# Kernel tuning notes

Hardware: AMD Instinct MI355X
Metric: run time of the kernel (lower is better)

Reference implementation:

```python
import jax, jax.numpy as jnp
import numpy as np

B = 65536
IN_F = 512
OUT_F = 256
NUM_GROUPS = 8
EPS = 1e-5


def setup_inputs() -> dict:
    key = jax.random.key(0)
    ks = jax.random.split(key, 6)
    return {
        "x": jax.random.normal(ks[0], (B, IN_F), dtype=jnp.float32),
        "weight": jax.random.normal(ks[1], (OUT_F, IN_F), dtype=jnp.float32) * 0.05,
        "bias_linear": jax.random.normal(ks[2], (OUT_F,), dtype=jnp.float32) * 0.05,
        "weight_gn": jax.random.normal(ks[3], (OUT_F,), dtype=jnp.float32),
        "bias_gn": jax.random.normal(ks[4], (OUT_F,), dtype=jnp.float32),
        "bias": jax.random.normal(ks[5], (1, OUT_F, 1, 1), dtype=jnp.float32),
    }


def reference(x, weight, bias_linear, weight_gn, bias_gn, bias):
    # Linear: (B, IN_F) @ (IN_F, OUT_F) + bias -> (B, OUT_F)
    h = jnp.einsum("bi,oi->bo", x, weight) + bias_linear
    # GroupNorm over channel dim (dim=1) with NUM_GROUPS groups
    g = h.reshape(B, NUM_GROUPS, OUT_F // NUM_GROUPS)
    mean = jnp.mean(g, axis=2, keepdims=True)
    var = jnp.mean(jnp.square(g - mean), axis=2, keepdims=True)
    gn = ((g - mean) * jax.lax.rsqrt(var + EPS)).reshape(B, OUT_F)
    gn = gn * weight_gn + bias_gn
    # Min over channels, keepdim -> (B, 1)
    min_vals = jnp.min(gn, axis=1, keepdims=True)
    # torch broadcasting: (B,1) + (1,256,1,1) -> (1,256,B,1)
    result = min_vals + bias
    return result
```

## Files before the change

kernel.cpp:

```cpp
#include <hip/hip_runtime.h>
#include <hip/hip_bf16.h>

#define B_ROWS 65536
#define K_DIM  512
#define N_DIM  256
#define EPS    1e-5f
#define MTILE  32
#define LDS_STRIDE 264

using short8  = __attribute__((ext_vector_type(8))) short;
using floatx4 = __attribute__((ext_vector_type(4))) float;

__device__ __forceinline__ unsigned short f2bf(float f) {
    unsigned u = __builtin_bit_cast(unsigned, f);
    u += 0x7FFFu + ((u >> 16) & 1u);
    return (unsigned short)(u >> 16);
}

__global__ __launch_bounds__(64) void pack_w(const float* __restrict__ W,
                                             unsigned short* __restrict__ P) {
    int b    = blockIdx.x;
    int nt   = b >> 4, kk = b & 15;
    int lane = threadIdx.x;
    int l15  = lane & 15, quad = lane >> 4;
    const float* src = W + (size_t)(nt * 16 + l15) * K_DIM + kk * 32 + quad * 8;
    short8 v;
#pragma unroll
    for (int j = 0; j < 8; ++j) v[j] = (short)f2bf(src[j]);
    *(short8*)(P + ((size_t)(nt * 16 + kk) * 64 + lane) * 8) = v;
}

__global__ __launch_bounds__(256, 6) void gemm_gn_min_bcast(
    const float* __restrict__ X, const unsigned short* __restrict__ P,
    const float* __restrict__ bias_lin, const float* __restrict__ wgn,
    const float* __restrict__ bgn, const float* __restrict__ bias,
    float* __restrict__ out)
{
    __shared__ unsigned short Ash[MTILE * LDS_STRIDE];
    __shared__ float sm_min[4][MTILE];
    __shared__ float m_sh[MTILE];

    const int tid  = threadIdx.x;
    const int wave = tid >> 6, lane = tid & 63;
    const int l15  = lane & 15, quad = lane >> 4;
    const size_t row0 = (size_t)blockIdx.x * MTILE;

    floatx4 acc[2][4] = {};

    for (int kh = 0; kh < 2; ++kh) {
        if (kh) __syncthreads();
        for (int i = tid; i < MTILE * 64; i += 256) {
            int r = i >> 6, c4 = (i & 63) << 2;
            const float4 f = *(const float4*)(X + (row0 + r) * K_DIM + kh * 256 + c4);
            ushort4 h;
            h.x = f2bf(f.x); h.y = f2bf(f.y); h.z = f2bf(f.z); h.w = f2bf(f.w);
            *(ushort4*)(&Ash[r * LDS_STRIDE + c4]) = h;
        }
        __syncthreads();

#pragma unroll
        for (int kk = 0; kk < 8; ++kk) {
            const int kkg = kh * 8 + kk;
            short8 a[2], b[4];
#pragma unroll
            for (int rt = 0; rt < 2; ++rt)
                a[rt] = *(const short8*)&Ash[(rt * 16 + l15) * LDS_STRIDE + kk * 32 + quad * 8];
#pragma unroll
            for (int ct = 0; ct < 4; ++ct) {
                int nt = wave * 4 + ct;
                b[ct] = *(const short8*)(P + (((size_t)nt * 16 + kkg) * 64 + lane) * 8);
            }
#pragma unroll
            for (int rt = 0; rt < 2; ++rt)
#pragma unroll
                for (int ct = 0; ct < 4; ++ct)
                    acc[rt][ct] = __builtin_amdgcn_mfma_f32_16x16x32_bf16(
                        a[rt], b[ct], acc[rt][ct], 0, 0, 0);
        }
    }

    float bl[4], wg[4], bg[4];
#pragma unroll
    for (int ct = 0; ct < 4; ++ct) {
        int col = wave * 64 + ct * 16 + l15;
        bl[ct] = bias_lin[col]; wg[ct] = wgn[col]; bg[ct] = bgn[col];
    }

#pragma unroll
    for (int rt = 0; rt < 2; ++rt) {
#pragma unroll
        for (int reg = 0; reg < 4; ++reg) {
            float v[4];
#pragma unroll
            for (int ct = 0; ct < 4; ++ct) v[ct] = acc[rt][ct][reg] + bl[ct];
            float rmin = 1e30f;
#pragma unroll
            for (int h = 0; h < 2; ++h) {
                float va = v[2 * h], vb = v[2 * h + 1];
                float s = va + vb, ss = va * va + vb * vb;
#pragma unroll
                for (int m = 1; m < 16; m <<= 1) {
                    s  += __shfl_xor(s, m);
                    ss += __shfl_xor(ss, m);
                }
                float mean = s * (1.0f / 32.0f);
                float var  = ss * (1.0f / 32.0f) - mean * mean;
                float inv  = rsqrtf(var + EPS);
                float ga = (va - mean) * inv * wg[2 * h]     + bg[2 * h];
                float gb = (vb - mean) * inv * wg[2 * h + 1] + bg[2 * h + 1];
                float mn = fminf(ga, gb);
#pragma unroll
                for (int m = 1; m < 16; m <<= 1) mn = fminf(mn, __shfl_xor(mn, m));
                rmin = fminf(rmin, mn);
            }
            if (l15 == 0) sm_min[wave][rt * 16 + quad * 4 + reg] = rmin;
        }
    }
    __syncthreads();
    if (tid < MTILE)
        m_sh[tid] = fminf(fminf(sm_min[0][tid], sm_min[1][tid]),
                          fminf(sm_min[2][tid], sm_min[3][tid]));
    __syncthreads();

    const int lane8 = tid & 7, cgrp = tid >> 3;
    float4 mv = *(const float4*)&m_sh[lane8 * 4];
#pragma unroll
    for (int pass = 0; pass < 8; ++pass) {
        int c = pass * 32 + cgrp;
        float bc = bias[c];
        float4 o;
        o.x = mv.x + bc; o.y = mv.y + bc; o.z = mv.z + bc; o.w = mv.w + bc;
        *(float4*)(out + (size_t)c * B_ROWS + row0 + lane8 * 4) = o;
    }
}

extern "C" void kernel_launch(void* const* d_in, const int* in_sizes, int n_in,
                              void* d_out, int out_size, void* d_ws, size_t ws_size,
                              hipStream_t stream) {
    const float* x    = (const float*)d_in[0];
    const float* w    = (const float*)d_in[1];
    const float* bl   = (const float*)d_in[2];
    const float* wg   = (const float*)d_in[3];
    const float* bg   = (const float*)d_in[4];
    const float* bias = (const float*)d_in[5];

    unsigned short* P = (unsigned short*)d_ws;
    float* out = (float*)d_out;

    hipLaunchKernelGGL(pack_w, dim3(256), dim3(64), 0, stream, w, P);
    hipLaunchKernelGGL(gemm_gn_min_bcast, dim3(B_ROWS / MTILE), dim3(256), 0, stream,
                       x, P, bl, wg, bg, bias, out);
}
```

Measured before the change: 260.2 us.

## Make fused GEMM-GroupNorm-min kernel persistent with register-resident weights and X prefetch

Replaces the one-block-per-tile launch with 256 persistent blocks of 512 threads that loop over row tiles. Each wave loads its slice of the packed bf16 weights into registers once, instead of re-reading them from global memory for every tile. The next tile's X rows are prefetched into registers while the current tile runs MFMA and the epilogue, and the full K=512 is staged in LDS at once. This is meant to remove repeated weight traffic and hide X load latency. The cost is heavy register pressure and only one large block per CU, so occupancy is low.

```diff
diff --git a/kernel.cpp b/kernel.cpp
--- a/kernel.cpp
+++ b/kernel.cpp
@@ -6,7 +6,8 @@
 #define N_DIM  256
 #define EPS    1e-5f
 #define MTILE  32
-#define LDS_STRIDE 264
+#define NBLK   256
+#define STRIDE 520
 
 using short8  = __attribute__((ext_vector_type(8))) short;
 using floatx4 = __attribute__((ext_vector_type(4))) float;
@@ -30,73 +31,84 @@
     *(short8*)(P + ((size_t)(nt * 16 + kk) * 64 + lane) * 8) = v;
 }
 
-__global__ __launch_bounds__(256, 6) void gemm_gn_min_bcast(
+__global__ __launch_bounds__(512, 2) void fused_persistent(
     const float* __restrict__ X, const unsigned short* __restrict__ P,
     const float* __restrict__ bias_lin, const float* __restrict__ wgn,
     const float* __restrict__ bgn, const float* __restrict__ bias,
     float* __restrict__ out)
 {
-    __shared__ unsigned short Ash[MTILE * LDS_STRIDE];
-    __shared__ float sm_min[4][MTILE];
+    __shared__ unsigned short Ash[MTILE * STRIDE];
+    __shared__ float sm_min[8][MTILE];
     __shared__ float m_sh[MTILE];
 
     const int tid  = threadIdx.x;
     const int wave = tid >> 6, lane = tid & 63;
     const int l15  = lane & 15, quad = lane >> 4;
-    const size_t row0 = (size_t)blockIdx.x * MTILE;
 
-    floatx4 acc[2][4] = {};
+    short8 bfr[2][16];
+#pragma unroll
+    for (int ct = 0; ct < 2; ++ct)
+#pragma unroll
+        for (int kkg = 0; kkg < 16; ++kkg) {
+            int nt = 2 * wave + ct;
+            bfr[ct][kkg] = *(const short8*)(P + (((size_t)nt * 16 + kkg) * 64 + lane) * 8);
+        }
 
-    for (int kh = 0; kh < 2; ++kh) {
-        if (kh) __syncthreads();
-        for (int i = tid; i < MTILE * 64; i += 256) {
-            int r = i >> 6, c4 = (i & 63) << 2;
-            const float4 f = *(const float4*)(X + (row0 + r) * K_DIM + kh * 256 + c4);
+    float bl[2], wg[2], bg[2];
+#pragma unroll
+    for (int ct = 0; ct < 2; ++ct) {
+        int col = wave * 32 + ct * 16 + l15;
+        bl[ct] = bias_lin[col]; wg[ct] = wgn[col]; bg[ct] = bgn[col];
+    }
+    float bias_r[4];
+#pragma unroll
+    for (int pass = 0; pass < 4; ++pass) bias_r[pass] = bias[pass * 64 + (tid >> 3)];
+
+    const int r0 = tid >> 7;
+    const int c4 = (tid & 127) * 4;
+
+    const int tiles = B_ROWS / MTILE;
+    int t = blockIdx.x;
+
+    float4 xq[8];
+#pragma unroll
+    for (int p = 0; p < 8; ++p)
+        xq[p] = *(const float4*)(X + (size_t)(t * MTILE + r0 + 4 * p) * K_DIM + c4);
+
+    for (; t < tiles; t += NBLK) {
+#pragma unroll
+        for (int p = 0; p < 8; ++p) {
             ushort4 h;
-            h.x = f2bf(f.x); h.y = f2bf(f.y); h.z = f2bf(f.z); h.w = f2bf(f.w);
-            *(ushort4*)(&Ash[r * LDS_STRIDE + c4]) = h;
+            h.x = f2bf(xq[p].x); h.y = f2bf(xq[p].y);
+            h.z = f2bf(xq[p].z); h.w = f2bf(xq[p].w);
+            *(ushort4*)(&Ash[(r0 + 4 * p) * STRIDE + c4]) = h;
         }
         __syncthreads();
 
+        int tn = t + NBLK;
+        if (tn < tiles) {
 #pragma unroll
-        for (int kk = 0; kk < 8; ++kk) {
-            const int kkg = kh * 8 + kk;
-            short8 a[2], b[4];
+            for (int p = 0; p < 8; ++p)
+                xq[p] = *(const float4*)(X + (size_t)(tn * MTILE + r0 + 4 * p) * K_DIM + c4);
+        }
+
+        floatx4 acc[2][2] = {};
 #pragma unroll
-            for (int rt = 0; rt < 2; ++rt)
-                a[rt] = *(const short8*)&Ash[(rt * 16 + l15) * LDS_STRIDE + kk * 32 + quad * 8];
-#pragma unroll
-            for (int ct = 0; ct < 4; ++ct) {
-                int nt = wave * 4 + ct;
-                b[ct] = *(const short8*)(P + (((size_t)nt * 16 + kkg) * 64 + lane) * 8);
-            }
-#pragma unroll
-            for (int rt = 0; rt < 2; ++rt)
-#pragma unroll
-                for (int ct = 0; ct < 4; ++ct)
-                    acc[rt][ct] = __builtin_amdgcn_mfma_f32_16x16x32_bf16(
-                        a[rt], b[ct], acc[rt][ct], 0, 0, 0);
+        for (int kk = 0; kk < 16; ++kk) {
+            short8 a0 = *(const short8*)&Ash[(l15)      * STRIDE + kk * 32 + quad * 8];
+            short8 a1 = *(const short8*)&Ash[(16 + l15) * STRIDE + kk * 32 + quad * 8];
+            acc[0][0] = __builtin_amdgcn_mfma_f32_16x16x32_bf16(a0, bfr[0][kk], acc[0][0], 0, 0, 0);
+            acc[0][1] = __builtin_amdgcn_mfma_f32_16x16x32_bf16(a0, bfr[1][kk], acc[0][1], 0, 0, 0);
+            acc[1][0] = __builtin_amdgcn_mfma_f32_16x16x32_bf16(a1, bfr[0][kk], acc[1][0], 0, 0, 0);
+            acc[1][1] = __builtin_amdgcn_mfma_f32_16x16x32_bf16(a1, bfr[1][kk], acc[1][1], 0, 0, 0);
         }
-    }
-
-    float bl[4], wg[4], bg[4];
-#pragma unroll
-    for (int ct = 0; ct < 4; ++ct) {
-        int col = wave * 64 + ct * 16 + l15;
-        bl[ct] = bias_lin[col]; wg[ct] = wgn[col]; bg[ct] = bgn[col];
-    }
 
 #pragma unroll
-    for (int rt = 0; rt < 2; ++rt) {
+        for (int rt = 0; rt < 2; ++rt) {
 #pragma unroll
-        for (int reg = 0; reg < 4; ++reg) {
-            float v[4];
-#pragma unroll
-            for (int ct = 0; ct < 4; ++ct) v[ct] = acc[rt][ct][reg] + bl[ct];
-            float rmin = 1e30f;
-#pragma unroll
-            for (int h = 0; h < 2; ++h) {
-                float va = v[2 * h], vb = v[2 * h + 1];
+            for (int reg = 0; reg < 4; ++reg) {
+                float va = acc[rt][0][reg] + bl[0];
+                float vb = acc[rt][1][reg] + bl[1];
                 float s = va + vb, ss = va * va + vb * vb;
 #pragma unroll
                 for (int m = 1; m < 16; m <<= 1) {
@@ -106,31 +118,32 @@
                 float mean = s * (1.0f / 32.0f);
                 float var  = ss * (1.0f / 32.0f) - mean * mean;
                 float inv  = rsqrtf(var + EPS);
-                float ga = (va - mean) * inv * wg[2 * h]     + bg[2 * h];
-                float gb = (vb - mean) * inv * wg[2 * h + 1] + bg[2 * h + 1];
+                float ga = (va - mean) * inv * wg[0] + bg[0];
+                float gb = (vb - mean) * inv * wg[1] + bg[1];
                 float mn = fminf(ga, gb);
 #pragma unroll
                 for (int m = 1; m < 16; m <<= 1) mn = fminf(mn, __shfl_xor(mn, m));
-                rmin = fminf(rmin, mn);
+                if (l15 == 0) sm_min[wave][rt * 16 + quad * 4 + reg] = mn;
             }
-            if (l15 == 0) sm_min[wave][rt * 16 + quad * 4 + reg] = rmin;
         }
-    }
-    __syncthreads();
-    if (tid < MTILE)
-        m_sh[tid] = fminf(fminf(sm_min[0][tid], sm_min[1][tid]),
-                          fminf(sm_min[2][tid], sm_min[3][tid]));
-    __syncthreads();
+        __syncthreads();
+        if (tid < MTILE) {
+            float m0 = sm_min[0][tid];
+#pragma unroll
+            for (int w = 1; w < 8; ++w) m0 = fminf(m0, sm_min[w][tid]);
+            m_sh[tid] = m0;
+        }
+        __syncthreads();
 
-    const int lane8 = tid & 7, cgrp = tid >> 3;
-    float4 mv = *(const float4*)&m_sh[lane8 * 4];
+        float4 mv = *(const float4*)&m_sh[(tid & 7) * 4];
 #pragma unroll
-    for (int pass = 0; pass < 8; ++pass) {
-        int c = pass * 32 + cgrp;
-        float bc = bias[c];
-        float4 o;
-        o.x = mv.x + bc; o.y = mv.y + bc; o.z = mv.z + bc; o.w = mv.w + bc;
-        *(float4*)(out + (size_t)c * B_ROWS + row0 + lane8 * 4) = o;
+        for (int pass = 0; pass < 4; ++pass) {
+            int c = pass * 64 + (tid >> 3);
+            float bc = bias_r[pass];
+            float4 o;
+            o.x = mv.x + bc; o.y = mv.y + bc; o.z = mv.z + bc; o.w = mv.w + bc;
+            *(float4*)(out + (size_t)c * B_ROWS + t * MTILE + (tid & 7) * 4) = o;
+        }
     }
 }
 
@@ -148,6 +161,6 @@
     float* out = (float*)d_out;
 
     hipLaunchKernelGGL(pack_w, dim3(256), dim3(64), 0, stream, w, P);
-    hipLaunchKernelGGL(gemm_gn_min_bcast, dim3(B_ROWS / MTILE), dim3(256), 0, stream,
+    hipLaunchKernelGGL(fused_persistent, dim3(NBLK), dim3(512), 0, stream,
                        x, P, bl, wg, bg, bias, out);
 }
```

Result: faster. 236.3 us (-9.2%).

## Use 8-wave blocks with register-resident B fragments and single-pass X staging

Applied to the files above, without the earlier changes.

Doubles the block to 512 threads (8 waves). Each wave now owns two 16-column N tiles, one from each of the two 16-column halves of its 32-channel group, and preloads all 16 K-step weight fragments for one tile into registers before running its MFMAs. The full 32x512 X tile is converted to bf16 and staged in LDS in one pass with wide loads, which removes the second staging round and its barrier. Each wave covers exactly one GroupNorm group, so the group sums need no cross-wave exchange. The cost is higher register pressure from the 16 short8 fragments, plus a larger LDS footprint and block size that may reduce occupancy.

```diff
diff --git a/kernel.cpp b/kernel.cpp
--- a/kernel.cpp
+++ b/kernel.cpp
@@ -3,10 +3,9 @@
 
 #define B_ROWS 65536
 #define K_DIM  512
-#define N_DIM  256
 #define EPS    1e-5f
 #define MTILE  32
-#define LDS_STRIDE 264
+#define XSTR   520
 
 using short8  = __attribute__((ext_vector_type(8))) short;
 using floatx4 = __attribute__((ext_vector_type(4))) float;
@@ -30,107 +29,123 @@
     *(short8*)(P + ((size_t)(nt * 16 + kk) * 64 + lane) * 8) = v;
 }
 
-__global__ __launch_bounds__(256, 6) void gemm_gn_min_bcast(
+__global__ __launch_bounds__(512, 4) void fused(
     const float* __restrict__ X, const unsigned short* __restrict__ P,
     const float* __restrict__ bias_lin, const float* __restrict__ wgn,
     const float* __restrict__ bgn, const float* __restrict__ bias,
     float* __restrict__ out)
 {
-    __shared__ unsigned short Ash[MTILE * LDS_STRIDE];
-    __shared__ float sm_min[4][MTILE];
+    __shared__ unsigned short Ash[MTILE * XSTR];
+    __shared__ float Msh[MTILE * 8];
     __shared__ float m_sh[MTILE];
 
     const int tid  = threadIdx.x;
     const int wave = tid >> 6, lane = tid & 63;
     const int l15  = lane & 15, quad = lane >> 4;
-    const size_t row0 = (size_t)blockIdx.x * MTILE;
+    const int t    = blockIdx.x;
+    const size_t row0 = (size_t)t * MTILE;
 
-    floatx4 acc[2][4] = {};
-
-    for (int kh = 0; kh < 2; ++kh) {
-        if (kh) __syncthreads();
-        for (int i = tid; i < MTILE * 64; i += 256) {
-            int r = i >> 6, c4 = (i & 63) << 2;
-            const float4 f = *(const float4*)(X + (row0 + r) * K_DIM + kh * 256 + c4);
-            ushort4 h;
-            h.x = f2bf(f.x); h.y = f2bf(f.y); h.z = f2bf(f.z); h.w = f2bf(f.w);
-            *(ushort4*)(&Ash[r * LDS_STRIDE + c4]) = h;
-        }
-        __syncthreads();
-
+    short8 bfr[16];
+    {
+        const unsigned short* p0 = P + (((size_t)(2 * wave) * 16) * 64 + lane) * 8;
 #pragma unroll
-        for (int kk = 0; kk < 8; ++kk) {
-            const int kkg = kh * 8 + kk;
-            short8 a[2], b[4];
-#pragma unroll
-            for (int rt = 0; rt < 2; ++rt)
-                a[rt] = *(const short8*)&Ash[(rt * 16 + l15) * LDS_STRIDE + kk * 32 + quad * 8];
-#pragma unroll
-            for (int ct = 0; ct < 4; ++ct) {
-                int nt = wave * 4 + ct;
-                b[ct] = *(const short8*)(P + (((size_t)nt * 16 + kkg) * 64 + lane) * 8);
-            }
-#pragma unroll
-            for (int rt = 0; rt < 2; ++rt)
-#pragma unroll
-                for (int ct = 0; ct < 4; ++ct)
-                    acc[rt][ct] = __builtin_amdgcn_mfma_f32_16x16x32_bf16(
-                        a[rt], b[ct], acc[rt][ct], 0, 0, 0);
-        }
+        for (int kk = 0; kk < 16; ++kk)
+            bfr[kk] = *(const short8*)(p0 + (size_t)kk * 64 * 8);
     }
 
-    float bl[4], wg[4], bg[4];
+    {
+        const int sr = tid >> 4, sc = tid & 15;
+        const float* xp = X + (row0 + sr) * K_DIM + sc * 32;
+        float4 f[8];
 #pragma unroll
-    for (int ct = 0; ct < 4; ++ct) {
-        int col = wave * 64 + ct * 16 + l15;
-        bl[ct] = bias_lin[col]; wg[ct] = wgn[col]; bg[ct] = bgn[col];
-    }
-
+        for (int p = 0; p < 8; ++p) f[p] = *(const float4*)(xp + p * 4);
 #pragma unroll
-    for (int rt = 0; rt < 2; ++rt) {
-#pragma unroll
-        for (int reg = 0; reg < 4; ++reg) {
-            float v[4];
-#pragma unroll
-            for (int ct = 0; ct < 4; ++ct) v[ct] = acc[rt][ct][reg] + bl[ct];
-            float rmin = 1e30f;
-#pragma unroll
-            for (int h = 0; h < 2; ++h) {
-                float va = v[2 * h], vb = v[2 * h + 1];
-                float s = va + vb, ss = va * va + vb * vb;
-#pragma unroll
-                for (int m = 1; m < 16; m <<= 1) {
-                    s  += __shfl_xor(s, m);
-                    ss += __shfl_xor(ss, m);
-                }
-                float mean = s * (1.0f / 32.0f);
-                float var  = ss * (1.0f / 32.0f) - mean * mean;
-                float inv  = rsqrtf(var + EPS);
-                float ga = (va - mean) * inv * wg[2 * h]     + bg[2 * h];
-                float gb = (vb - mean) * inv * wg[2 * h + 1] + bg[2 * h + 1];
-                float mn = fminf(ga, gb);
-#pragma unroll
-                for (int m = 1; m < 16; m <<= 1) mn = fminf(mn, __shfl_xor(mn, m));
-                rmin = fminf(rmin, mn);
-            }
-            if (l15 == 0) sm_min[wave][rt * 16 + quad * 4 + reg] = rmin;
+        for (int pq = 0; pq < 4; ++pq) {
+            short8 v;
+            v[0] = (short)f2bf(f[2*pq].x);   v[1] = (short)f2bf(f[2*pq].y);
+            v[2] = (short)f2bf(f[2*pq].z);   v[3] = (short)f2bf(f[2*pq].w);
+            v[4] = (short)f2bf(f[2*pq+1].x); v[5] = (short)f2bf(f[2*pq+1].y);
+            v[6] = (short)f2bf(f[2*pq+1].z); v[7] = (short)f2bf(f[2*pq+1].w);
+            *(short8*)&Ash[sr * XSTR + sc * 32 + pq * 8] = v;
         }
     }
     __syncthreads();
-    if (tid < MTILE)
-        m_sh[tid] = fminf(fminf(sm_min[0][tid], sm_min[1][tid]),
-                          fminf(sm_min[2][tid], sm_min[3][tid]));
+
+    floatx4 accA0 = {0.f,0.f,0.f,0.f}, accA1 = {0.f,0.f,0.f,0.f};
+#pragma unroll
+    for (int kk = 0; kk < 16; ++kk) {
+        short8 a0 = *(const short8*)&Ash[l15 * XSTR + kk * 32 + quad * 8];
+        short8 a1 = *(const short8*)&Ash[(16 + l15) * XSTR + kk * 32 + quad * 8];
+        accA0 = __builtin_amdgcn_mfma_f32_16x16x32_bf16(a0, bfr[kk], accA0, 0, 0, 0);
+        accA1 = __builtin_amdgcn_mfma_f32_16x16x32_bf16(a1, bfr[kk], accA1, 0, 0, 0);
+    }
+    __builtin_amdgcn_sched_barrier(0);
+
+    {
+        const unsigned short* p1 = P + (((size_t)(2 * wave + 1) * 16) * 64 + lane) * 8;
+#pragma unroll
+        for (int kk = 0; kk < 16; ++kk)
+            bfr[kk] = *(const short8*)(p1 + (size_t)kk * 64 * 8);
+    }
+    floatx4 accB0 = {0.f,0.f,0.f,0.f}, accB1 = {0.f,0.f,0.f,0.f};
+#pragma unroll
+    for (int kk = 0; kk < 16; ++kk) {
+        short8 a0 = *(const short8*)&Ash[l15 * XSTR + kk * 32 + quad * 8];
+        short8 a1 = *(const short8*)&Ash[(16 + l15) * XSTR + kk * 32 + quad * 8];
+        accB0 = __builtin_amdgcn_mfma_f32_16x16x32_bf16(a0, bfr[kk], accB0, 0, 0, 0);
+        accB1 = __builtin_amdgcn_mfma_f32_16x16x32_bf16(a1, bfr[kk], accB1, 0, 0, 0);
+    }
+
+    const int c0 = wave * 32 + l15, c1 = c0 + 16;
+    const float bl0 = bias_lin[c0], bl1 = bias_lin[c1];
+    const float wg0 = wgn[c0], wg1 = wgn[c1];
+    const float bg0 = bgn[c0], bg1 = bgn[c1];
+
+#pragma unroll
+    for (int rs = 0; rs < 2; ++rs) {
+        floatx4 aA = rs ? accA1 : accA0;
+        floatx4 aB = rs ? accB1 : accB0;
+#pragma unroll
+        for (int reg = 0; reg < 4; ++reg) {
+            float va = aA[reg] + bl0;
+            float vb = aB[reg] + bl1;
+            float s = va + vb, ss = va * va + vb * vb;
+#pragma unroll
+            for (int m = 1; m < 16; m <<= 1) {
+                s  += __shfl_xor(s, m);
+                ss += __shfl_xor(ss, m);
+            }
+            float mean = s * (1.0f / 32.0f);
+            float var  = ss * (1.0f / 32.0f) - mean * mean;
+            float inv  = rsqrtf(var + EPS);
+            float ga = (va - mean) * inv * wg0 + bg0;
+            float gb = (vb - mean) * inv * wg1 + bg1;
+            float mn = fminf(ga, gb);
+#pragma unroll
+            for (int m = 1; m < 16; m <<= 1) mn = fminf(mn, __shfl_xor(mn, m));
+            if (l15 == 0) Msh[(rs * 16 + quad * 4 + reg) * 8 + wave] = mn;
+        }
+    }
+    __syncthreads();
+    if (tid < MTILE) {
+        float m0 = Msh[tid * 8 + 0];
+#pragma unroll
+        for (int g = 1; g < 8; ++g) m0 = fminf(m0, Msh[tid * 8 + g]);
+        m_sh[tid] = m0;
+    }
     __syncthreads();
 
-    const int lane8 = tid & 7, cgrp = tid >> 3;
-    float4 mv = *(const float4*)&m_sh[lane8 * 4];
+    {
+        float4 mv = *(const float4*)&m_sh[(tid & 7) * 4];
+        const int cb = tid >> 3;
 #pragma unroll
-    for (int pass = 0; pass < 8; ++pass) {
-        int c = pass * 32 + cgrp;
-        float bc = bias[c];
-        float4 o;
-        o.x = mv.x + bc; o.y = mv.y + bc; o.z = mv.z + bc; o.w = mv.w + bc;
-        *(float4*)(out + (size_t)c * B_ROWS + row0 + lane8 * 4) = o;
+        for (int j = 0; j < 4; ++j) {
+            int c = cb + 64 * j;
+            float bc = bias[c];
+            float4 o;
+            o.x = mv.x + bc; o.y = mv.y + bc; o.z = mv.z + bc; o.w = mv.w + bc;
+            *(float4*)(out + (size_t)c * B_ROWS + row0 + (tid & 7) * 4) = o;
+        }
     }
 }
 
@@ -148,6 +163,6 @@
     float* out = (float*)d_out;
 
     hipLaunchKernelGGL(pack_w, dim3(256), dim3(64), 0, stream, w, P);
-    hipLaunchKernelGGL(gemm_gn_min_bcast, dim3(B_ROWS / MTILE), dim3(256), 0, stream,
+    hipLaunchKernelGGL(fused, dim3(B_ROWS / MTILE), dim3(512), 0, stream,
                        x, P, bl, wg, bg, bias, out);
 }
```

Result: slower. 272.7 us (+4.8%).

## Give each wave full-width 16-row tiles, drop LDS staging and block syncs

Applied to the files above, without the earlier changes.

Restructures the fused GEMM+GroupNorm+min kernel so each wave computes all 256 output columns for its own 16 rows. X is read directly from global memory into MFMA A-fragments rather than staged through LDS, and the cross-wave min reduction through shared memory and barriers goes away. Per-channel parameters are packed into one float4 array by a new small kernel, so they load with one access each. The intent is to remove LDS traffic and block synchronisation. The cost is many more accumulator registers per wave (lower occupancy, launch bounds now 3), uncoalesced strided X loads, and every wave reading all of packed W from cache.

```diff
diff --git a/kernel.cpp b/kernel.cpp
--- a/kernel.cpp
+++ b/kernel.cpp
@@ -3,10 +3,7 @@
 
 #define B_ROWS 65536
 #define K_DIM  512
-#define N_DIM  256
 #define EPS    1e-5f
-#define MTILE  32
-#define LDS_STRIDE 264
 
 using short8  = __attribute__((ext_vector_type(8))) short;
 using floatx4 = __attribute__((ext_vector_type(4))) float;
@@ -30,107 +27,85 @@
     *(short8*)(P + ((size_t)(nt * 16 + kk) * 64 + lane) * 8) = v;
 }
 
-__global__ __launch_bounds__(256, 6) void gemm_gn_min_bcast(
+__global__ __launch_bounds__(256) void pack_prm(
+    const float* __restrict__ bl, const float* __restrict__ wg,
+    const float* __restrict__ bg, const float* __restrict__ bias,
+    float* __restrict__ PRM) {
+    int c = threadIdx.x;
+    float4 p;
+    p.x = bl[c]; p.y = wg[c]; p.z = bg[c]; p.w = bias[c];
+    *(float4*)(PRM + c * 4) = p;
+}
+
+__global__ __launch_bounds__(256, 3) void fused(
     const float* __restrict__ X, const unsigned short* __restrict__ P,
-    const float* __restrict__ bias_lin, const float* __restrict__ wgn,
-    const float* __restrict__ bgn, const float* __restrict__ bias,
-    float* __restrict__ out)
+    const float* __restrict__ PRM, float* __restrict__ out)
 {
-    __shared__ unsigned short Ash[MTILE * LDS_STRIDE];
-    __shared__ float sm_min[4][MTILE];
-    __shared__ float m_sh[MTILE];
-
     const int tid  = threadIdx.x;
     const int wave = tid >> 6, lane = tid & 63;
     const int l15  = lane & 15, quad = lane >> 4;
-    const size_t row0 = (size_t)blockIdx.x * MTILE;
+    const size_t row0 = ((size_t)blockIdx.x * 4 + wave) * 16;
 
-    floatx4 acc[2][4] = {};
+    const float* xrow = X + (row0 + l15) * K_DIM;
 
-    for (int kh = 0; kh < 2; ++kh) {
-        if (kh) __syncthreads();
-        for (int i = tid; i < MTILE * 64; i += 256) {
-            int r = i >> 6, c4 = (i & 63) << 2;
-            const float4 f = *(const float4*)(X + (row0 + r) * K_DIM + kh * 256 + c4);
-            ushort4 h;
-            h.x = f2bf(f.x); h.y = f2bf(f.y); h.z = f2bf(f.z); h.w = f2bf(f.w);
-            *(ushort4*)(&Ash[r * LDS_STRIDE + c4]) = h;
-        }
-        __syncthreads();
+    floatx4 acc[16];
+#pragma unroll
+    for (int ct = 0; ct < 16; ++ct) acc[ct] = (floatx4){0.f, 0.f, 0.f, 0.f};
 
 #pragma unroll
-        for (int kk = 0; kk < 8; ++kk) {
-            const int kkg = kh * 8 + kk;
-            short8 a[2], b[4];
+    for (int kk = 0; kk < 16; ++kk) {
+        float4 f0 = *(const float4*)(xrow + kk * 32 + quad * 8);
+        float4 f1 = *(const float4*)(xrow + kk * 32 + quad * 8 + 4);
+        short8 a;
+        a[0] = (short)f2bf(f0.x); a[1] = (short)f2bf(f0.y);
+        a[2] = (short)f2bf(f0.z); a[3] = (short)f2bf(f0.w);
+        a[4] = (short)f2bf(f1.x); a[5] = (short)f2bf(f1.y);
+        a[6] = (short)f2bf(f1.z); a[7] = (short)f2bf(f1.w);
 #pragma unroll
-            for (int rt = 0; rt < 2; ++rt)
-                a[rt] = *(const short8*)&Ash[(rt * 16 + l15) * LDS_STRIDE + kk * 32 + quad * 8];
-#pragma unroll
-            for (int ct = 0; ct < 4; ++ct) {
-                int nt = wave * 4 + ct;
-                b[ct] = *(const short8*)(P + (((size_t)nt * 16 + kkg) * 64 + lane) * 8);
-            }
-#pragma unroll
-            for (int rt = 0; rt < 2; ++rt)
-#pragma unroll
-                for (int ct = 0; ct < 4; ++ct)
-                    acc[rt][ct] = __builtin_amdgcn_mfma_f32_16x16x32_bf16(
-                        a[rt], b[ct], acc[rt][ct], 0, 0, 0);
+        for (int ct = 0; ct < 16; ++ct) {
+            short8 b = *(const short8*)(P + (((size_t)ct * 16 + kk) * 64 + lane) * 8);
+            acc[ct] = __builtin_amdgcn_mfma_f32_16x16x32_bf16(a, b, acc[ct], 0, 0, 0);
         }
     }
 
-    float bl[4], wg[4], bg[4];
+    float4 prm[16];
 #pragma unroll
-    for (int ct = 0; ct < 4; ++ct) {
-        int col = wave * 64 + ct * 16 + l15;
-        bl[ct] = bias_lin[col]; wg[ct] = wgn[col]; bg[ct] = bgn[col];
+    for (int ct = 0; ct < 16; ++ct)
+        prm[ct] = *(const float4*)(PRM + (size_t)(ct * 16 + l15) * 4);
+
+    float rmin[4];
+#pragma unroll
+    for (int reg = 0; reg < 4; ++reg) {
+        float gmin = 1e30f;
+#pragma unroll
+        for (int g = 0; g < 8; ++g) {
+            float va = acc[2 * g][reg]     + prm[2 * g].x;
+            float vb = acc[2 * g + 1][reg] + prm[2 * g + 1].x;
+            float s = va + vb, ss = va * va + vb * vb;
+#pragma unroll
+            for (int m = 1; m < 16; m <<= 1) {
+                s  += __shfl_xor(s, m);
+                ss += __shfl_xor(ss, m);
+            }
+            float mean = s * (1.0f / 32.0f);
+            float var  = ss * (1.0f / 32.0f) - mean * mean;
+            float inv  = rsqrtf(var + EPS);
+            float ga = (va - mean) * inv * prm[2 * g].y     + prm[2 * g].z;
+            float gb = (vb - mean) * inv * prm[2 * g + 1].y + prm[2 * g + 1].z;
+            gmin = fminf(gmin, fminf(ga, gb));
+        }
+#pragma unroll
+        for (int m = 1; m < 16; m <<= 1) gmin = fminf(gmin, __shfl_xor(gmin, m));
+        rmin[reg] = gmin;
     }
 
 #pragma unroll
-    for (int rt = 0; rt < 2; ++rt) {
-#pragma unroll
-        for (int reg = 0; reg < 4; ++reg) {
-            float v[4];
-#pragma unroll
-            for (int ct = 0; ct < 4; ++ct) v[ct] = acc[rt][ct][reg] + bl[ct];
-            float rmin = 1e30f;
-#pragma unroll
-            for (int h = 0; h < 2; ++h) {
-                float va = v[2 * h], vb = v[2 * h + 1];
-                float s = va + vb, ss = va * va + vb * vb;
-#pragma unroll
-                for (int m = 1; m < 16; m <<= 1) {
-                    s  += __shfl_xor(s, m);
-                    ss += __shfl_xor(ss, m);
-                }
-                float mean = s * (1.0f / 32.0f);
-                float var  = ss * (1.0f / 32.0f) - mean * mean;
-                float inv  = rsqrtf(var + EPS);
-                float ga = (va - mean) * inv * wg[2 * h]     + bg[2 * h];
-                float gb = (vb - mean) * inv * wg[2 * h + 1] + bg[2 * h + 1];
-                float mn = fminf(ga, gb);
-#pragma unroll
-                for (int m = 1; m < 16; m <<= 1) mn = fminf(mn, __shfl_xor(mn, m));
-                rmin = fminf(rmin, mn);
-            }
-            if (l15 == 0) sm_min[wave][rt * 16 + quad * 4 + reg] = rmin;
-        }
-    }
-    __syncthreads();
-    if (tid < MTILE)
-        m_sh[tid] = fminf(fminf(sm_min[0][tid], sm_min[1][tid]),
-                          fminf(sm_min[2][tid], sm_min[3][tid]));
-    __syncthreads();
-
-    const int lane8 = tid & 7, cgrp = tid >> 3;
-    float4 mv = *(const float4*)&m_sh[lane8 * 4];
-#pragma unroll
-    for (int pass = 0; pass < 8; ++pass) {
-        int c = pass * 32 + cgrp;
-        float bc = bias[c];
+    for (int ct = 0; ct < 16; ++ct) {
+        float bc = prm[ct].w;
         float4 o;
-        o.x = mv.x + bc; o.y = mv.y + bc; o.z = mv.z + bc; o.w = mv.w + bc;
-        *(float4*)(out + (size_t)c * B_ROWS + row0 + lane8 * 4) = o;
+        o.x = rmin[0] + bc; o.y = rmin[1] + bc;
+        o.z = rmin[2] + bc; o.w = rmin[3] + bc;
+        *(float4*)(out + (size_t)(ct * 16 + l15) * B_ROWS + row0 + quad * 4) = o;
     }
 }
 
@@ -144,10 +119,11 @@
     const float* bg   = (const float*)d_in[4];
     const float* bias = (const float*)d_in[5];
 
-    unsigned short* P = (unsigned short*)d_ws;
+    unsigned short* P   = (unsigned short*)d_ws;
+    float*          PRM = (float*)((char*)d_ws + 256 * 1024);
     float* out = (float*)d_out;
 
     hipLaunchKernelGGL(pack_w, dim3(256), dim3(64), 0, stream, w, P);
-    hipLaunchKernelGGL(gemm_gn_min_bcast, dim3(B_ROWS / MTILE), dim3(256), 0, stream,
-                       x, P, bl, wg, bg, bias, out);
+    hipLaunchKernelGGL(pack_prm, dim3(1), dim3(256), 0, stream, bl, wg, bg, bias, PRM);
+    hipLaunchKernelGGL(fused, dim3(B_ROWS / 64), dim3(256), 0, stream, x, P, PRM, out);
 }
```

New measurement: 337.9 us. +29.9%, slower.
